# Kernel tuning notes

Measured on AMD Instinct MI355X. Metric: run time of the kernel, lower is better.

## Reference

```python
import jax, jax.numpy as jnp
import numpy as np

TEMPERATURE = 0.07
HARD_K = 10
N, D, NUM_CLASSES = 8192, 256, 128


def setup_inputs() -> dict:
    key = jax.random.key(0)
    kf, kl = jax.random.split(key)
    feats = jax.random.normal(kf, (N, D), dtype=jnp.float32)
    labels = jax.random.randint(kl, (N,), 0, NUM_CLASSES, dtype=jnp.int64)
    return {"feats": feats, "labels": labels}


def _loss(feats, labels):
    n = feats.shape[0]
    # F.normalize(dim=-1) with eps=1e-12
    norm = jnp.maximum(jnp.linalg.norm(feats, axis=-1, keepdims=True), 1e-12)
    z = feats / norm
    sim = (z @ z.T) / TEMPERATURE  # [N, N]

    same = labels[:, None] == labels[None, :]
    eye = jnp.eye(n, dtype=bool)
    same_ns = same & ~eye          # same label, excluding self
    diff = ~same                   # different label

    neg_inf = jnp.float32(-jnp.inf)
    # uniform random positive per row via Gumbel-max over the same-label mask
    g = jax.random.gumbel(jax.random.key(42), (n, n), dtype=jnp.float32)
    pos_idx = jnp.argmax(jnp.where(same_ns, g, neg_inf), axis=1)  # [N]
    pos_logit = jnp.take_along_axis(sim, pos_idx[:, None], axis=1)[:, 0]

    # hard negatives: top-k of sims over different-label columns
    neg_sims = jnp.where(diff, sim, neg_inf)
    hard_vals, _ = jax.lax.top_k(neg_sims, HARD_K)  # [N, K]; exp(-inf)=0 handles rows with <K negatives

    num = jnp.exp(pos_logit)
    den = num + jnp.sum(jnp.exp(hard_vals), axis=1)
    li = -jnp.log(jnp.maximum(num / jnp.maximum(den, 1e-8), 1e-8))

    valid = jnp.any(same_ns, axis=1) & jnp.any(diff, axis=1)
    cnt = jnp.maximum(jnp.sum(valid), 1)
    return jnp.sum(jnp.where(valid, li, 0.0)) / cnt.astype(li.dtype)


def reference(feats, labels):
    return _loss(feats, labels)
```

## Files before the change

### kernel.cpp

```cpp
#include <hip/hip_runtime.h>
#include <cstdint>
#include <math.h>

#define N_     8192
#define D_     256
#define NLBL   128
#define TEMP_INV 14.285714285714286f
#define HARDK  10
#define THETA  0.16f
#define GCAP   256

#define NCHUNK 64
#define CHUNK  (N_ / NCHUNK)
#define TILES  (CHUNK / 32)
#define CSLOT  8

typedef __attribute__((ext_vector_type(8)))  short bf16x8;
typedef __attribute__((ext_vector_type(16))) float f32x16;

__device__ __forceinline__ uint32_t rotl32(uint32_t x, int n) {
  return (x << n) | (x >> (32 - n));
}
__device__ uint32_t tf_bits(uint32_t idx) {
  uint32_t x0 = 0u, x1 = idx;
  const uint32_t k0 = 0u, k1 = 42u;
  const uint32_t k2 = k0 ^ k1 ^ 0x1BD11BDAu;
  x0 += k0; x1 += k1;
#define TFR(r) { x0 += x1; x1 = rotl32(x1, r); x1 ^= x0; }
  TFR(13) TFR(15) TFR(26) TFR(6)
  x0 += k1; x1 += k2 + 1u;
  TFR(17) TFR(29) TFR(16) TFR(24)
  x0 += k2; x1 += k0 + 2u;
  TFR(13) TFR(15) TFR(26) TFR(6)
  x0 += k0; x1 += k1 + 3u;
  TFR(17) TFR(29) TFR(16) TFR(24)
  x0 += k1; x1 += k2 + 4u;
  TFR(13) TFR(15) TFR(26) TFR(6)
  x0 += k2; x1 += k0 + 5u;
#undef TFR
  return x0 ^ x1;
}

__device__ __forceinline__ uint32_t f2bf(float x) {
  uint32_t b = __float_as_uint(x);
  return (b + 0x7FFFu + ((b >> 16) & 1u)) >> 16;
}

__global__ __launch_bounds__(256) void prep_group_kernel(
    const float* __restrict__ feats, const int* __restrict__ labels,
    float* __restrict__ inv_norm, unsigned short* __restrict__ zt,
    uint32_t* __restrict__ mask_g, int* __restrict__ glist, int* __restrict__ cnt_g) {
  __shared__ uint4 tile[16][33];
  __shared__ int lcnt;
  const int tid = threadIdx.x;

  if (blockIdx.x < 512) {
    const int row0 = blockIdx.x * 16;
    const int wv = tid >> 6, l = tid & 63;
#pragma unroll
    for (int rr = 0; rr < 4; ++rr) {
      const int rloc = wv * 4 + rr;
      const int row = row0 + rloc;
      float4 v = ((const float4*)feats)[(size_t)row * 64 + l];
      float ss = v.x * v.x + v.y * v.y + v.z * v.z + v.w * v.w;
#pragma unroll
      for (int o = 32; o; o >>= 1) ss += __shfl_xor(ss, o);
      float inv = 1.0f / fmaxf(sqrtf(ss), 1e-12f);
      if (l == 0) inv_norm[row] = inv;
      uint2 p;
      p.x = f2bf(v.x * inv) | (f2bf(v.y * inv) << 16);
      p.y = f2bf(v.z * inv) | (f2bf(v.w * inv) << 16);
      *(uint2*)((char*)&tile[0][0] + rloc * 528 + l * 8) = p;
    }
    __syncthreads();
#pragma unroll
    for (int it = 0; it < 2; ++it) {
      int idx = it * 256 + tid;
      int c = idx >> 4, r = idx & 15;
      ((uint4*)zt)[(size_t)c * N_ + row0 + r] = tile[r][c];
    }
  } else {
    const int b = blockIdx.x - 512;
    const int lane = tid & 63, wv = tid >> 6;
    if (tid == 0) lcnt = 0;
    __syncthreads();
    for (int it = 0; it < N_; it += 256) {
      int col = it + tid;
      bool pred = (labels[col] == b);
      unsigned long long m = __ballot(pred);
      if (lane == 0) {
        int w0 = (it + wv * 64) >> 5;
        mask_g[b * 256 + w0]     = (uint32_t)m;
        mask_g[b * 256 + w0 + 1] = (uint32_t)(m >> 32);
      }
      if (pred) {
        int p = atomicAdd(&lcnt, 1);
        if (p < GCAP) glist[b * GCAP + p] = col;
      }
    }
    __syncthreads();
    if (tid == 0) cnt_g[b] = lcnt;
  }
}

__device__ __forceinline__ void stage_tile(const unsigned short* zt, char (*AbK)[1024],
                                           int colT, int wid, int l, int kg) {
  const char* base = (const char*)zt + ((size_t)kg * N_ + colT + (l & 31)) * 16;
#pragma unroll
  for (int q = 0; q < 4; ++q) {
    const int kk = wid * 4 + q;
    __builtin_amdgcn_global_load_lds(
        (const __attribute__((address_space(1))) void*)(base + (size_t)kk * (2 * N_ * 16)),
        (__attribute__((address_space(3))) void*)(&AbK[kk][0]), 16, 0, 0);
  }
}

#define INS8(H0,H1,H2,H3,H4,H5,H6,H7,POS,C) \
  { H0 = (POS==0)?(C):H0; H1 = (POS==1)?(C):H1; H2 = (POS==2)?(C):H2; H3 = (POS==3)?(C):H3; \
    H4 = (POS==4)?(C):H4; H5 = (POS==5)?(C):H5; H6 = (POS==6)?(C):H6; H7 = (POS==7)?(C):H7; \
    ++POS; }

__global__ __launch_bounds__(256) void collect_kernel(const unsigned short* __restrict__ zt,
                                                      const int* __restrict__ labels,
                                                      const uint32_t* __restrict__ mask_g,
                                                      float* __restrict__ vals,
                                                      int* __restrict__ counts) {
  __shared__ char Ab[2][16][1024];
  __shared__ float mcell[128 * 8];
  __shared__ int   mcnt[128];

  const int tid = threadIdx.x;
  const int l = tid & 63, wid = tid >> 6;
  const int kg = l >> 5;

  int rc = 0, rem = blockIdx.x;
  while (rem >= NCHUNK - rc) { rem -= NCHUNK - rc; ++rc; }
  const int cc = rc + rem;
  const bool offdiag = (cc > rc);

  const int row0 = rc * 128;
  const int col0 = cc * CHUNK;
  const int rowW = row0 + wid * 32 + (l & 31);
  const int lab = labels[rowW];

  if (tid < 128) mcnt[tid] = 0;

  uint32_t mW[TILES];
  {
    uint4 m0 = *(const uint4*)(mask_g + lab * 256 + (col0 >> 5));
    mW[0] = m0.x; mW[1] = m0.y; mW[2] = m0.z; mW[3] = m0.w;
  }

  bf16x8 bf[16];
  {
    const uint4* ztq = (const uint4*)zt;
#pragma unroll
    for (int kk = 0; kk < 16; ++kk)
      bf[kk] = *(const bf16x8*)&ztq[(size_t)(kk * 2 + kg) * N_ + rowW];
  }

  float h0=0,h1=0,h2=0,h3=0,h4=0,h5=0,h6=0,h7=0;
  int pos = 0;
  float* vb = vals + ((size_t)rowW * NCHUNK + cc) * CSLOT;

  stage_tile(zt, Ab[0], col0, wid, l, kg);
  __syncthreads();

  int buf = 0;
#pragma unroll
  for (int t = 0; t < TILES; ++t) {
    if (t + 1 < TILES) stage_tile(zt, Ab[buf ^ 1], col0 + (t + 1) * 32, wid, l, kg);

    f32x16 acc;
#pragma unroll
    for (int r = 0; r < 16; ++r) acc[r] = 0.f;
    __builtin_amdgcn_s_setprio(1);
#pragma unroll
    for (int kk = 0; kk < 16; ++kk) {
      bf16x8 a = *(const bf16x8*)&Ab[buf][kk][l * 16];
      acc = __builtin_amdgcn_mfma_f32_32x32x16_bf16(a, bf[kk], acc, 0, 0, 0);
    }
    __builtin_amdgcn_s_setprio(0);

    const uint32_t wsh = mW[t] >> (kg * 4);
#pragma unroll
    for (int r = 0; r < 16; ++r) {
      const int cpos = (r & 3) + 8 * (r >> 2);
      bool hit = ((((wsh >> cpos) & 1u) == 0u) && (acc[r] > THETA));
      if (__any(hit)) {
        if (hit) {
          INS8(h0,h1,h2,h3,h4,h5,h6,h7, pos, acc[r]);
          if (offdiag) {
            int jc = t * 32 + cpos + 4 * kg;
            int p = atomicAdd(&mcnt[jc], 1);
            if (p < 8) mcell[jc * 8 + p] = acc[r];
          }
        }
      }
    }
    __syncthreads();
    buf ^= 1;
  }

  if (kg == 0) {
    if (pos > 0) vb[0] = h0;  if (pos > 1) vb[1] = h1;
    if (pos > 2) vb[2] = h2;  if (pos > 3) vb[3] = h3;
    if (pos > 4) vb[4] = h4;  if (pos > 5) vb[5] = h5;
    if (pos > 6) vb[6] = h6;  if (pos > 7) vb[7] = h7;
  } else {
    if (pos > 0) vb[7] = h0;  if (pos > 1) vb[6] = h1;
    if (pos > 2) vb[5] = h2;  if (pos > 3) vb[4] = h3;
    if (pos > 4) vb[3] = h4;  if (pos > 5) vb[2] = h5;
    if (pos > 6) vb[1] = h6;  if (pos > 7) vb[0] = h7;
  }
  counts[(rowW * NCHUNK + cc) * 2 + kg] = pos;

  if (offdiag) {
    int jc = tid >> 1, half = tid & 1;
    float4 m = *(float4*)&mcell[jc * 8 + half * 4];
    float* dm = vals + ((size_t)(col0 + jc) * NCHUNK + rc) * CSLOT + half * 4;
    *(float4*)dm = m;
    if (half == 0) {
      counts[((col0 + jc) * NCHUNK + rc) * 2 + 0] = mcnt[jc];
      counts[((col0 + jc) * NCHUNK + rc) * 2 + 1] = 0;
    }
  }
}

__global__ __launch_bounds__(256) void finalize_kernel(
    const float* __restrict__ feats, const int* __restrict__ labels,
    const float* __restrict__ inv_norm,
    const int* __restrict__ glist, const int* __restrict__ cnt_g,
    const int* __restrict__ counts, const float* __restrict__ vals,
    float* __restrict__ li, int* __restrict__ valid) {
  const int row = blockIdx.x * 4 + (threadIdx.x >> 6);
  const int lane = threadIdx.x & 63;
  const int lab = labels[row];
  const int gc = cnt_g[lab];
  const int gn = gc < GCAP ? gc : GCAP;
  const float4* feats4 = (const float4*)feats;

  uint32_t bk = 0u; int bj = -1;
  for (int e = lane; e < gn; e += 64) {
    int j = glist[lab * GCAP + e];
    if (j != row) {
      uint32_t key = tf_bits((uint32_t)row * (uint32_t)N_ + (uint32_t)j) >> 9;
      if (bj < 0 || key > bk || (key == bk && j < bj)) { bk = key; bj = j; }
    }
  }
#pragma unroll
  for (int o = 32; o; o >>= 1) {
    uint32_t ok = __shfl_xor(bk, o);
    int oj = __shfl_xor(bj, o);
    if (oj >= 0 && (bj < 0 || ok > bk || (ok == bk && oj < bj))) { bk = ok; bj = oj; }
  }

  float pc = 0.f;
  if (bj >= 0) {
    float4 a = feats4[(size_t)row * 64 + lane];
    float4 b = feats4[(size_t)bj * 64 + lane];
    float p = a.x * b.x + a.y * b.y + a.z * b.z + a.w * b.w;
#pragma unroll
    for (int o = 32; o; o >>= 1) p += __shfl_xor(p, o);
    pc = p * inv_norm[row] * inv_norm[bj];
  }

  float vv[8];
  int ovf = 0;
#pragma unroll
  for (int q = 0; q < 8; ++q) {
    int s = lane + 64 * q;
    int cell = s >> 3, wi = s & 7;
    int c0 = counts[(row * NCHUNK + cell) * 2 + 0];
    int c1 = counts[(row * NCHUNK + cell) * 2 + 1];
    ovf |= (c0 + c1 > CSLOT) ? 1 : 0;
    float val = vals[(size_t)row * (NCHUNK * CSLOT) + s];
    int c1b = c1 < CSLOT ? c1 : CSLOT;
    bool live = (wi < c0) || (wi >= CSLOT - c1b);
    vv[q] = live ? val : -INFINITY;
  }

  float num = expf(pc * TEMP_INV);
  float den = num;
  int got = 0;
#pragma unroll 1
  for (int it = 0; it < HARDK; ++it) {
    float lm = fmaxf(fmaxf(fmaxf(vv[0], vv[1]), fmaxf(vv[2], vv[3])),
                     fmaxf(fmaxf(vv[4], vv[5]), fmaxf(vv[6], vv[7])));
    float wm = lm;
#pragma unroll
    for (int o = 32; o; o >>= 1) wm = fmaxf(wm, __shfl_xor(wm, o));
    if (wm < -1e37f) break;
    den += expf(wm * TEMP_INV);
    ++got;
    unsigned long long b = __ballot(lm == wm);
    int fl = __ffsll((long long)b) - 1;
    if (lane == fl) {
      if      (vv[0] == wm) vv[0] = -INFINITY;
      else if (vv[1] == wm) vv[1] = -INFINITY;
      else if (vv[2] == wm) vv[2] = -INFINITY;
      else if (vv[3] == wm) vv[3] = -INFINITY;
      else if (vv[4] == wm) vv[4] = -INFINITY;
      else if (vv[5] == wm) vv[5] = -INFINITY;
      else if (vv[6] == wm) vv[6] = -INFINITY;
      else                  vv[7] = -INFINITY;
    }
  }

  const int ndiff = N_ - gc;
  const bool vld = (bj >= 0) && (ndiff > 0);
  const int want = ndiff < HARDK ? ndiff : HARDK;

  if (vld && (__any(ovf) || got < want)) {
    float tk[HARDK];
#pragma unroll
    for (int k = 0; k < HARDK; ++k) tk[k] = -INFINITY;
    const float invr = inv_norm[row];
    const float4 a = feats4[(size_t)row * 64 + lane];
#pragma unroll 1
    for (int j = 0; j < N_; ++j) {
      if (j == row || labels[j] == lab) continue;
      float4 b = feats4[(size_t)j * 64 + lane];
      float p = a.x * b.x + a.y * b.y + a.z * b.z + a.w * b.w;
#pragma unroll
      for (int o = 32; o; o >>= 1) p += __shfl_xor(p, o);
      float c = p * invr * inv_norm[j];
      if (c > tk[0]) {
        tk[0] = c;
#pragma unroll
        for (int q = 0; q < HARDK - 1; ++q)
          if (tk[q] > tk[q + 1]) { float tmp = tk[q]; tk[q] = tk[q + 1]; tk[q + 1] = tmp; }
      }
    }
    den = num;
#pragma unroll
    for (int k = 0; k < HARDK; ++k)
      if (tk[k] > -1e37f) den += expf(tk[k] * TEMP_INV);
  }

  float L = 0.f;
  if (vld) L = -logf(fmaxf(num / fmaxf(den, 1e-8f), 1e-8f));
  if (lane == 0) {
    li[row] = L;
    valid[row] = vld ? 1 : 0;
  }
}

__global__ __launch_bounds__(256) void reduce_kernel(const float* __restrict__ li,
                                                     const int* __restrict__ valid,
                                                     float* __restrict__ out) {
  __shared__ float ssum[4];
  __shared__ int scnt[4];
  float s = 0.f; int c = 0;
  for (int i = threadIdx.x; i < N_; i += 256) { s += li[i]; c += valid[i]; }
#pragma unroll
  for (int o = 32; o; o >>= 1) { s += __shfl_down(s, o); c += __shfl_down(c, o); }
  if ((threadIdx.x & 63) == 0) { ssum[threadIdx.x >> 6] = s; scnt[threadIdx.x >> 6] = c; }
  __syncthreads();
  if (threadIdx.x == 0) {
    float S = 0.f; int C = 0;
    for (int w = 0; w < 4; ++w) { S += ssum[w]; C += scnt[w]; }
    out[0] = S / (float)(C > 0 ? C : 1);
  }
}

extern "C" void kernel_launch(void* const* d_in, const int* in_sizes, int n_in,
                              void* d_out, int out_size, void* d_ws, size_t ws_size,
                              hipStream_t stream) {
  const float* feats  = (const float*)d_in[0];
  const int*   labels = (const int*)d_in[1];
  float* out = (float*)d_out;

  char* w = (char*)d_ws;
  unsigned short* zt  = (unsigned short*)w;  w += (size_t)N_ * D_ * 2;
  float* inv_norm = (float*)w;               w += (size_t)N_ * 4;
  uint32_t* mask_g = (uint32_t*)w;           w += (size_t)NLBL * 256 * 4;
  int* glist = (int*)w;                      w += (size_t)NLBL * GCAP * 4;
  int* cnt_g = (int*)w;                      w += (size_t)NLBL * 4;
  int* counts = (int*)w;                     w += (size_t)N_ * NCHUNK * 2 * 4;
  float* vals = (float*)w;                   w += (size_t)N_ * NCHUNK * CSLOT * 4;
  float* li_arr = (float*)w;                 w += (size_t)N_ * 4;
  int* valid_arr = (int*)w;                  w += (size_t)N_ * 4;

  hipLaunchKernelGGL(prep_group_kernel, dim3(640), dim3(256), 0, stream,
                     feats, labels, inv_norm, zt, mask_g, glist, cnt_g);
  hipLaunchKernelGGL(collect_kernel, dim3((NCHUNK * (NCHUNK + 1)) / 2), dim3(256), 0, stream,
                     zt, labels, mask_g, vals, counts);
  hipLaunchKernelGGL(finalize_kernel, dim3(N_ / 4), dim3(256), 0, stream,
                     feats, labels, inv_norm, glist, cnt_g, counts, vals, li_arr, valid_arr);
  hipLaunchKernelGGL(reduce_kernel, dim3(1), dim3(256), 0, stream, li_arr, valid_arr, out);
}
```

Measured before the change: 85.20 us.

## Single-buffer LDS tiles, swizzle block order, use nontemporal output stores

Replaces the double-buffered LDS staging of column tiles with a single buffer that is refilled after each tile's compute, with an extra barrier. This halves LDS use so more blocks can be resident per CU. It also remaps block IDs so consecutive blocks are spread across the triangular work list, likely to balance work across XCDs. Output stores to vals and counts become nontemporal, which avoids polluting cache. The cost is that the load and MFMA work inside a block no longer overlap.

```diff
diff --git a/kernel.cpp b/kernel.cpp
--- a/kernel.cpp
+++ b/kernel.cpp
@@ -14,6 +14,7 @@
 #define CHUNK  (N_ / NCHUNK)
 #define TILES  (CHUNK / 32)
 #define CSLOT  8
+#define NTRI   ((NCHUNK * (NCHUNK + 1)) / 2)
 
 typedef __attribute__((ext_vector_type(8)))  short bf16x8;
 typedef __attribute__((ext_vector_type(16))) float f32x16;
@@ -125,7 +126,7 @@
                                                       const uint32_t* __restrict__ mask_g,
                                                       float* __restrict__ vals,
                                                       int* __restrict__ counts) {
-  __shared__ char Ab[2][16][1024];
+  __shared__ char Ab[16][1024];
   __shared__ float mcell[128 * 8];
   __shared__ int   mcnt[128];
 
@@ -133,7 +134,9 @@
   const int l = tid & 63, wid = tid >> 6;
   const int kg = l >> 5;
 
-  int rc = 0, rem = blockIdx.x;
+  const int bid = (blockIdx.x & 7) * (NTRI / 8) + (blockIdx.x >> 3);
+
+  int rc = 0, rem = bid;
   while (rem >= NCHUNK - rc) { rem -= NCHUNK - rc; ++rc; }
   const int cc = rc + rem;
   const bool offdiag = (cc > rc);
@@ -163,21 +166,18 @@
   int pos = 0;
   float* vb = vals + ((size_t)rowW * NCHUNK + cc) * CSLOT;
 
-  stage_tile(zt, Ab[0], col0, wid, l, kg);
+  stage_tile(zt, Ab, col0, wid, l, kg);
   __syncthreads();
 
-  int buf = 0;
 #pragma unroll
   for (int t = 0; t < TILES; ++t) {
-    if (t + 1 < TILES) stage_tile(zt, Ab[buf ^ 1], col0 + (t + 1) * 32, wid, l, kg);
-
     f32x16 acc;
 #pragma unroll
     for (int r = 0; r < 16; ++r) acc[r] = 0.f;
     __builtin_amdgcn_s_setprio(1);
 #pragma unroll
     for (int kk = 0; kk < 16; ++kk) {
-      bf16x8 a = *(const bf16x8*)&Ab[buf][kk][l * 16];
+      bf16x8 a = *(const bf16x8*)&Ab[kk][l * 16];
       acc = __builtin_amdgcn_mfma_f32_32x32x16_bf16(a, bf[kk], acc, 0, 0, 0);
     }
     __builtin_amdgcn_s_setprio(0);
@@ -199,30 +199,44 @@
       }
     }
     __syncthreads();
-    buf ^= 1;
+    if (t + 1 < TILES) {
+      stage_tile(zt, Ab, col0 + (t + 1) * 32, wid, l, kg);
+      __syncthreads();
+    }
   }
 
   if (kg == 0) {
-    if (pos > 0) vb[0] = h0;  if (pos > 1) vb[1] = h1;
-    if (pos > 2) vb[2] = h2;  if (pos > 3) vb[3] = h3;
-    if (pos > 4) vb[4] = h4;  if (pos > 5) vb[5] = h5;
-    if (pos > 6) vb[6] = h6;  if (pos > 7) vb[7] = h7;
+    if (pos > 0) __builtin_nontemporal_store(h0, vb + 0);
+    if (pos > 1) __builtin_nontemporal_store(h1, vb + 1);
+    if (pos > 2) __builtin_nontemporal_store(h2, vb + 2);
+    if (pos > 3) __builtin_nontemporal_store(h3, vb + 3);
+    if (pos > 4) __builtin_nontemporal_store(h4, vb + 4);
+    if (pos > 5) __builtin_nontemporal_store(h5, vb + 5);
+    if (pos > 6) __builtin_nontemporal_store(h6, vb + 6);
+    if (pos > 7) __builtin_nontemporal_store(h7, vb + 7);
   } else {
-    if (pos > 0) vb[7] = h0;  if (pos > 1) vb[6] = h1;
-    if (pos > 2) vb[5] = h2;  if (pos > 3) vb[4] = h3;
-    if (pos > 4) vb[3] = h4;  if (pos > 5) vb[2] = h5;
-    if (pos > 6) vb[1] = h6;  if (pos > 7) vb[0] = h7;
-  }
-  counts[(rowW * NCHUNK + cc) * 2 + kg] = pos;
+    if (pos > 0) __builtin_nontemporal_store(h0, vb + 7);
+    if (pos > 1) __builtin_nontemporal_store(h1, vb + 6);
+    if (pos > 2) __builtin_nontemporal_store(h2, vb + 5);
+    if (pos > 3) __builtin_nontemporal_store(h3, vb + 4);
+    if (pos > 4) __builtin_nontemporal_store(h4, vb + 3);
+    if (pos > 5) __builtin_nontemporal_store(h5, vb + 2);
+    if (pos > 6) __builtin_nontemporal_store(h6, vb + 1);
+    if (pos > 7) __builtin_nontemporal_store(h7, vb + 0);
+  }
+  __builtin_nontemporal_store(pos, counts + (rowW * NCHUNK + cc) * 2 + kg);
 
   if (offdiag) {
     int jc = tid >> 1, half = tid & 1;
     float4 m = *(float4*)&mcell[jc * 8 + half * 4];
     float* dm = vals + ((size_t)(col0 + jc) * NCHUNK + rc) * CSLOT + half * 4;
-    *(float4*)dm = m;
+    __builtin_nontemporal_store(m.x, dm + 0);
+    __builtin_nontemporal_store(m.y, dm + 1);
+    __builtin_nontemporal_store(m.z, dm + 2);
+    __builtin_nontemporal_store(m.w, dm + 3);
     if (half == 0) {
-      counts[((col0 + jc) * NCHUNK + rc) * 2 + 0] = mcnt[jc];
-      counts[((col0 + jc) * NCHUNK + rc) * 2 + 1] = 0;
+      __builtin_nontemporal_store(mcnt[jc], counts + ((col0 + jc) * NCHUNK + rc) * 2 + 0);
+      __builtin_nontemporal_store(0,        counts + ((col0 + jc) * NCHUNK + rc) * 2 + 1);
     }
   }
 }
@@ -384,7 +398,7 @@
 
   hipLaunchKernelGGL(prep_group_kernel, dim3(640), dim3(256), 0, stream,
                      feats, labels, inv_norm, zt, mask_g, glist, cnt_g);
-  hipLaunchKernelGGL(collect_kernel, dim3((NCHUNK * (NCHUNK + 1)) / 2), dim3(256), 0, stream,
+  hipLaunchKernelGGL(collect_kernel, dim3(NTRI), dim3(256), 0, stream,
                      zt, labels, mask_g, vals, counts);
   hipLaunchKernelGGL(finalize_kernel, dim3(N_ / 4), dim3(256), 0, stream,
                      feats, labels, inv_norm, glist, cnt_g, counts, vals, li_arr, valid_arr);
```

New measurement: 96.33 us. 1.13x slower.
